# Kernel optimization log

Measured on AMD Instinct MI355X. Metric: run time of the kernel, lower is better.

Reference implementation:

```python
import jax, jax.numpy as jnp
import numpy as np

N, E, IN_D, H, OUT_D = 50000, 800000, 128, 64, 64


def setup_inputs() -> dict:
    key = jax.random.key(0)
    ks = jax.random.split(key, 16)
    s = lambda k, shape: jax.random.normal(k, shape, dtype=jnp.float32) * (1.0 / np.sqrt(shape[0]))
    return {
        "x": jax.random.normal(ks[0], (N, IN_D), dtype=jnp.float32),
        "edge_index": jax.random.randint(ks[1], (2, E), 0, N, dtype=jnp.int32),
        "W1": s(ks[2], (IN_D, H)), "b1": jnp.zeros((H,), jnp.float32),
        "W2": s(ks[3], (H, 2 * H)), "b2": jnp.zeros((2 * H,), jnp.float32),
        "W3": s(ks[4], (2 * H, 4 * H)), "b3": jnp.zeros((4 * H,), jnp.float32),
        "dec1_w": s(ks[5], (4 * H, 2 * H, 2)), "dec1_b": jnp.zeros((2 * H,), jnp.float32),
        "dec2_w": s(ks[6], (2 * H, H, 2)), "dec2_b": jnp.zeros((H,), jnp.float32),
        "dec3_w": s(ks[7], (H, H, 2)), "dec3_b": jnp.zeros((H,), jnp.float32),
        "skip1_w": s(ks[8], (2 * H, 2 * H)), "skip1_b": jnp.zeros((2 * H,), jnp.float32),
        "skip2_w": s(ks[9], (H, H)), "skip2_b": jnp.zeros((H,), jnp.float32),
        "fin_w": s(ks[10], (OUT_D, 8 * H)), "fin_b": jnp.zeros((OUT_D,), jnp.float32),
    }


def _deconv2(x, w, b):
    # ConvTranspose1d(kernel=2, stride=2): [n,c,l] x [c,o,2] -> [n,o,2l]
    y = jnp.einsum('ncl,cok->nolk', x, w)
    n, o = x.shape[0], w.shape[1]
    return y.reshape(n, o, -1) + b[None, :, None]


def reference(x, edge_index, W1, b1, W2, b2, W3, b3, dec1_w, dec1_b, dec2_w, dec2_b,
              dec3_w, dec3_b, skip1_w, skip1_b, skip2_w, skip2_b, fin_w, fin_b):
    n = x.shape[0]
    loop = jnp.arange(n, dtype=edge_index.dtype)
    src = jnp.concatenate([edge_index[0], loop])
    tgt = jnp.concatenate([edge_index[1], loop])
    deg = jax.ops.segment_sum(jnp.ones_like(src, dtype=x.dtype), tgt, num_segments=n)
    dinv = jax.lax.rsqrt(deg)  # deg >= 1 due to self-loops
    norm = dinv[src] * dinv[tgt]  # [E+N]

    def gcn(h, W, b):
        hw = h @ W
        agg = jax.ops.segment_sum(hw[src] * norm[:, None], tgt, num_segments=n)
        return agg + b

    x1 = jax.nn.gelu(gcn(x, W1, b1))    # [N, H]
    x2 = jax.nn.gelu(gcn(x1, W2, b2))   # [N, 2H]
    x3 = jax.nn.gelu(gcn(x2, W3, b3))   # [N, 4H]

    d = _deconv2(x3[:, :, None], dec1_w, dec1_b)           # [N, 2H, 2]
    d = d + (x2 @ skip1_w.T + skip1_b)[:, :, None]
    d = _deconv2(d, dec2_w, dec2_b)                        # [N, H, 4]
    d = d + (x1 @ skip2_w.T + skip2_b)[:, :, None]
    d = _deconv2(d, dec3_w, dec3_b)                        # [N, H, 8]
    out = d.reshape(n, -1) @ fin_w.T + fin_b               # [N, OUT_D]
    return out
```

## Files before the change

kernel.cpp:

```cpp
#include <hip/hip_runtime.h>
#include <hip/hip_bf16.h>

typedef __attribute__((ext_vector_type(8))) short short8_t;
typedef __attribute__((ext_vector_type(4))) float f32x4;

#define CAP 64

__device__ __forceinline__ float gelu_f(float x) {
    float x3 = x * x * x;
    return 0.5f * x * (1.0f + tanhf(0.7978845608028654f * (x + 0.044715f * x3)));
}
__device__ __forceinline__ float b2f(unsigned short u) {
    union { float f; unsigned int i; } c; c.i = ((unsigned int)u) << 16; return c.f;
}
__device__ __forceinline__ unsigned short f2bu(float f) {
    union { float f; unsigned int i; } c; c.f = f;
    unsigned int r = c.i + 0x7fffu + ((c.i >> 16) & 1u);
    return (unsigned short)(r >> 16);
}


__device__ __forceinline__ void d_EF(int bid, int t, const float* __restrict__ dec3_w,
                                     const float* __restrict__ fin_w, float* __restrict__ EF) {
    int i2 = bid * 4 + (t >> 6), od = t & 63;
    int c3 = i2 >> 2, pp = i2 & 3;
    const float* d3 = dec3_w + c3 * 128;
    const float* fw = fin_w + od * 512;
    float s = 0.f;
    #pragma unroll
    for (int o3 = 0; o3 < 64; ++o3) {
        s += d3[o3 * 2 + 0] * fw[o3 * 8 + pp * 2 + 0];
        s += d3[o3 * 2 + 1] * fw[o3 * 8 + pp * 2 + 1];
    }
    EF[i2 * 64 + od] = s;
}

__device__ __forceinline__ void d_CEF(int bid, int t, const float* __restrict__ dec2_w,
                                      const float* __restrict__ EF, float* __restrict__ CEF) {
    int i1 = bid * 4 + (t >> 6), od = t & 63;
    int c2 = i1 >> 1, lp = i1 & 1;
    const float* d2 = dec2_w + c2 * 128;
    float s = 0.f;
    #pragma unroll
    for (int o2 = 0; o2 < 64; ++o2) {
        s += d2[o2 * 2 + 0] * EF[(o2 * 4 + lp * 2 + 0) * 64 + od];
        s += d2[o2 * 2 + 1] * EF[(o2 * 4 + lp * 2 + 1) * 64 + od];
    }
    CEF[i1 * 64 + od] = s;
}

__device__ __forceinline__ void d_comp(int sb, int od,
                       const float* __restrict__ dec1_w, const float* __restrict__ skip1_w,
                       const float* __restrict__ skip2_w,
                       const float* __restrict__ dec1_b, const float* __restrict__ skip1_b,
                       const float* __restrict__ dec2_b, const float* __restrict__ skip2_b,
                       const float* __restrict__ dec3_b, const float* __restrict__ fin_w,
                       const float* __restrict__ fin_b,
                       const float* __restrict__ CEF, const float* __restrict__ EF,
                       unsigned short* __restrict__ McatT, float* __restrict__ m0) {
    if (sb < 256) {
        const float* d1 = dec1_w + sb * 256;
        float s = 0.f;
        for (int j = 0; j < 256; ++j) s += d1[j] * CEF[j * 64 + od];
        McatT[od * 448 + sb] = f2bu(s);
    } else if (sb < 384) {
        int c = sb - 256;
        float s = 0.f;
        for (int j = 0; j < 256; ++j) s += skip1_w[(j >> 1) * 128 + c] * CEF[j * 64 + od];
        McatT[od * 448 + sb] = f2bu(s);
    } else if (sb < 448) {
        int c = sb - 384;
        float s = 0.f;
        for (int j = 0; j < 256; ++j) s += skip2_w[(j >> 2) * 64 + c] * EF[j * 64 + od];
        McatT[od * 448 + sb] = f2bu(s);
    } else {
        float s = fin_b[od];
        for (int j = 0; j < 256; ++j) s += (dec1_b[j >> 1] + skip1_b[j >> 1]) * CEF[j * 64 + od];
        for (int j = 0; j < 256; ++j) s += (dec2_b[j >> 2] + skip2_b[j >> 2]) * EF[j * 64 + od];
        for (int j = 0; j < 512; ++j) s += dec3_b[j >> 3] * fin_w[od * 512 + j];
        m0[od] = s;
    }
}

__device__ __forceinline__ void d_wconv(int bid, int t,
                        const float* __restrict__ W1, const float* __restrict__ W2,
                        const float* __restrict__ W3,
                        unsigned short* __restrict__ W1T, unsigned short* __restrict__ W2T,
                        unsigned short* __restrict__ W3T) {
    int i = bid * 256 + t;
    if (i < 8192) {
        int k = i >> 6, n = i & 63;
        W1T[n * 128 + k] = f2bu(W1[i]);
    } else if (i < 16384) {
        int j = i - 8192; int k = j >> 7, n = j & 127;
        W2T[n * 64 + k] = f2bu(W2[j]);
    } else if (i < 49152) {
        int j = i - 16384; int k = j >> 8, n = j & 255;
        W3T[n * 128 + k] = f2bu(W3[j]);
    }
}

__device__ __forceinline__ void d_fillx(int bid, int t, const int* __restrict__ src,
                                        const int* __restrict__ tgt, int E,
                                        int* __restrict__ cnt, int* __restrict__ csr) {
    int i = (bid * 256 + t) * 8;
    if (i + 7 < E) {
        int4 t0 = *(const int4*)(tgt + i);
        int4 t1 = *(const int4*)(tgt + i + 4);
        int4 s0 = *(const int4*)(src + i);
        int4 s1 = *(const int4*)(src + i + 4);
        int k0 = atomicAdd(&cnt[t0.x], 1);
        int k1 = atomicAdd(&cnt[t0.y], 1);
        int k2 = atomicAdd(&cnt[t0.z], 1);
        int k3 = atomicAdd(&cnt[t0.w], 1);
        int k4 = atomicAdd(&cnt[t1.x], 1);
        int k5 = atomicAdd(&cnt[t1.y], 1);
        int k6 = atomicAdd(&cnt[t1.z], 1);
        int k7 = atomicAdd(&cnt[t1.w], 1);
        if (k0 < CAP) csr[(t0.x << 6) + k0] = s0.x;
        if (k1 < CAP) csr[(t0.y << 6) + k1] = s0.y;
        if (k2 < CAP) csr[(t0.z << 6) + k2] = s0.z;
        if (k3 < CAP) csr[(t0.w << 6) + k3] = s0.w;
        if (k4 < CAP) csr[(t1.x << 6) + k4] = s1.x;
        if (k5 < CAP) csr[(t1.y << 6) + k5] = s1.y;
        if (k6 < CAP) csr[(t1.z << 6) + k6] = s1.z;
        if (k7 < CAP) csr[(t1.w << 6) + k7] = s1.w;
    } else {
        for (int k = i; k < E; ++k) {
            int tt = tgt[k];
            int kk = atomicAdd(&cnt[tt], 1);
            if (kk < CAP) csr[(tt << 6) + kk] = src[k];
        }
    }
}

template<bool A32, bool BIAS, bool GELU, bool OUT32>
__device__ __forceinline__ void d_gmm(
    int bx, int by,
    const unsigned short* __restrict__ A, const float* __restrict__ Af, int lda,
    const unsigned short* __restrict__ Bt,
    const float* __restrict__ bias,
    void* __restrict__ Cv, int ldc, int M, int K) {
    constexpr int LDS_R = 72;
    __shared__ unsigned short As[64 * LDS_R];
    __shared__ unsigned short Bs[64 * LDS_R];
    const int tid = threadIdx.x;
    const int r0 = bx * 64, c0 = by * 64;
    const int w = tid >> 6, lane = tid & 63;
    const int wm = (w >> 1) * 32, wn = (w & 1) * 32;
    const int fr = lane & 15, kg = lane >> 4;
    f32x4 acc[2][2];
    #pragma unroll
    for (int m = 0; m < 2; ++m)
        #pragma unroll
        for (int n = 0; n < 2; ++n) { f32x4 z = {0.f, 0.f, 0.f, 0.f}; acc[m][n] = z; }

    const int sr = tid >> 2, sc = (tid & 3) * 16;
    const bool aok = (r0 + sr) < M;
    const unsigned short* ag = A32 ? nullptr : (A + (size_t)(r0 + sr) * lda + sc);
    const float* agf = A32 ? (Af + (size_t)(r0 + sr) * lda + sc) : nullptr;
    const unsigned short* bg = Bt + (size_t)(c0 + sr) * K + sc;

    for (int kt = 0; kt < K; kt += 64) {
        if (aok) {
            if constexpr (A32) {
                float4 f0 = *(const float4*)(agf + kt);
                float4 f1 = *(const float4*)(agf + kt + 4);
                float4 f2 = *(const float4*)(agf + kt + 8);
                float4 f3 = *(const float4*)(agf + kt + 12);
                unsigned short o[16] = { f2bu(f0.x), f2bu(f0.y), f2bu(f0.z), f2bu(f0.w),
                                         f2bu(f1.x), f2bu(f1.y), f2bu(f1.z), f2bu(f1.w),
                                         f2bu(f2.x), f2bu(f2.y), f2bu(f2.z), f2bu(f2.w),
                                         f2bu(f3.x), f2bu(f3.y), f2bu(f3.z), f2bu(f3.w) };
                *(uint4*)&As[sr * LDS_R + sc]     = ((const uint4*)o)[0];
                *(uint4*)&As[sr * LDS_R + sc + 8] = ((const uint4*)o)[1];
            } else {
                *(uint4*)&As[sr * LDS_R + sc]     = *(const uint4*)(ag + kt);
                *(uint4*)&As[sr * LDS_R + sc + 8] = *(const uint4*)(ag + kt + 8);
            }
        }
        *(uint4*)&Bs[sr * LDS_R + sc]     = *(const uint4*)(bg + kt);
        *(uint4*)&Bs[sr * LDS_R + sc + 8] = *(const uint4*)(bg + kt + 8);
        __syncthreads();
        #pragma unroll
        for (int s2 = 0; s2 < 2; ++s2) {
            short8_t afr[2], bfr[2];
            #pragma unroll
            for (int n = 0; n < 2; ++n)
                bfr[n] = *(const short8_t*)&Bs[(wn + n * 16 + fr) * LDS_R + s2 * 32 + kg * 8];
            #pragma unroll
            for (int m = 0; m < 2; ++m)
                afr[m] = *(const short8_t*)&As[(wm + m * 16 + fr) * LDS_R + s2 * 32 + kg * 8];
            #pragma unroll
            for (int m = 0; m < 2; ++m)
                #pragma unroll
                for (int n = 0; n < 2; ++n)
                    acc[m][n] = __builtin_amdgcn_mfma_f32_16x16x32_bf16(afr[m], bfr[n], acc[m][n], 0, 0, 0);
        }
        __syncthreads();
    }
    #pragma unroll
    for (int m = 0; m < 2; ++m) {
        #pragma unroll
        for (int n = 0; n < 2; ++n) {
            #pragma unroll
            for (int j = 0; j < 4; ++j) {
                int row = r0 + wm + m * 16 + kg * 4 + j;
                int col = c0 + wn + n * 16 + fr;
                if (row < M) {
                    float xv = acc[m][n][j];
                    if (BIAS) xv += bias[col];
                    if (GELU) xv = gelu_f(xv);
                    if (OUT32) ((float*)Cv)[(size_t)row * ldc + col] = xv;
                    else ((unsigned short*)Cv)[(size_t)row * ldc + col] = f2bu(xv);
                }
            }
        }
    }
}

template<int F, int LPN, bool FIRST, bool EPI>
__device__ __forceinline__ void d_aggb(
    int bid,
    const unsigned short* __restrict__ hin, int ldi,
    const int* __restrict__ cnt, const int* __restrict__ csr,
    float* __restrict__ normf,
    const float* __restrict__ bias,
    unsigned short* __restrict__ out, int ldo, int N) {
    constexpr int SLOTS = 64 / LPN;
    static_assert(F / LPN == 8, "V must be 8");
    int lane = threadIdx.x & 63;
    int v = bid * 4 + (threadIdx.x >> 6);
    if (v >= N) return;
    int slot = lane / LPN, fl = lane % LPN;
    int fo = fl * 8;
    int deg = cnt[v];
    float dv = rsqrtf((float)(deg + 1));
    int cntE = min(deg, CAP) + 1;
    int base = v << 6;
    float acc[8] = {};
    const unsigned short* hbase = hin + fo;
    int j = slot;
    for (; j + SLOTS < cntE; j += 2 * SLOTS) {
        int e0 = base + j - 1, e1 = base + j + SLOTS - 1;
        int u0 = (j == 0) ? v : csr[e0];
        int u1 = csr[e1];
        float w0, w1;
        if constexpr (FIRST) {
            w0 = (j == 0) ? dv * dv : rsqrtf((float)(cnt[u0] + 1)) * dv;
            w1 = rsqrtf((float)(cnt[u1] + 1)) * dv;
            if (fl == 0) {
                if (j > 0) normf[e0] = w0;
                normf[e1] = w1;
            }
        } else {
            w0 = (j == 0) ? dv * dv : normf[e0];
            w1 = normf[e1];
        }
        uint4 t0 = *(const uint4*)(hbase + (size_t)u0 * ldi);
        uint4 t1 = *(const uint4*)(hbase + (size_t)u1 * ldi);
        const unsigned short* a0 = (const unsigned short*)&t0;
        const unsigned short* a1 = (const unsigned short*)&t1;
        #pragma unroll
        for (int q = 0; q < 8; ++q) acc[q] = fmaf(b2f(a0[q]), w0, acc[q]);
        #pragma unroll
        for (int q = 0; q < 8; ++q) acc[q] = fmaf(b2f(a1[q]), w1, acc[q]);
    }
    if (j < cntE) {
        int e = base + j - 1;
        int u = (j == 0) ? v : csr[e];
        float wgt;
        if constexpr (FIRST) {
            wgt = (j == 0) ? dv * dv : rsqrtf((float)(cnt[u] + 1)) * dv;
            if (fl == 0 && j > 0) normf[e] = wgt;
        } else {
            wgt = (j == 0) ? dv * dv : normf[e];
        }
        uint4 t = *(const uint4*)(hbase + (size_t)u * ldi);
        const unsigned short* ts = (const unsigned short*)&t;
        #pragma unroll
        for (int q = 0; q < 8; ++q) acc[q] = fmaf(b2f(ts[q]), wgt, acc[q]);
    }
    #pragma unroll
    for (int off = LPN; off < 64; off <<= 1)
        #pragma unroll
        for (int q = 0; q < 8; ++q) acc[q] += __shfl_xor(acc[q], off, 64);
    if (slot == 0) {
        unsigned short o[8];
        #pragma unroll
        for (int q = 0; q < 8; ++q) {
            float xv = acc[q];
            if (EPI) xv = gelu_f(xv + bias[fo + q]);
            o[q] = f2bu(xv);
        }
        *(uint4*)(out + (size_t)v * ldo + fo) = *(const uint4*)o;
    }
}


template<bool A32, bool BIAS, bool GELU, bool OUT32>
__global__ __launch_bounds__(256) void k_gmm(
    const unsigned short* __restrict__ A, const float* __restrict__ Af, int lda,
    const unsigned short* __restrict__ Bt,
    const float* __restrict__ bias,
    void* __restrict__ Cv, int ldc, int M, int K) {
    d_gmm<A32, BIAS, GELU, OUT32>(blockIdx.x, blockIdx.y, A, Af, lda, Bt, bias, Cv, ldc, M, K);
}

template<int F, int LPN, bool FIRST, bool EPI>
__global__ __launch_bounds__(256) void k_aggb(
    const unsigned short* __restrict__ hin, int ldi,
    const int* __restrict__ cnt, const int* __restrict__ csr,
    float* __restrict__ normf, const float* __restrict__ bias,
    unsigned short* __restrict__ out, int ldo, int N) {
    d_aggb<F, LPN, FIRST, EPI>(blockIdx.x, hin, ldi, cnt, csr, normf, bias, out, ldo, N);
}

__global__ __launch_bounds__(256) void k_mega0(
    const float* __restrict__ W1, const float* __restrict__ W2, const float* __restrict__ W3,
    unsigned short* __restrict__ W1T, unsigned short* __restrict__ W2T,
    unsigned short* __restrict__ W3T,
    const float* __restrict__ dec3_w, const float* __restrict__ fin_w, float* __restrict__ EF,
    int* __restrict__ cnt, int N) {
    int b = blockIdx.x, t = threadIdx.x;
    if (b < 192) d_wconv(b, t, W1, W2, W3, W1T, W2T, W3T);
    else if (b < 256) d_EF(b - 192, t, dec3_w, fin_w, EF);
    else { int i = (b - 256) * 256 + t; if (i < N) cnt[i] = 0; }
}

__global__ __launch_bounds__(256) void k_megaA(
    const int* __restrict__ src, const int* __restrict__ tgt, int E,
    int* __restrict__ cnt, int* __restrict__ csr, int nf,
    const float* __restrict__ x, const unsigned short* __restrict__ W1T,
    unsigned short* __restrict__ hw1, int M, int ng,
    const float* __restrict__ dec2_w, const float* __restrict__ EF, float* __restrict__ CEF) {
    int b = blockIdx.x;
    if (b < nf)
        d_fillx(b, threadIdx.x, src, tgt, E, cnt, csr);
    else if (b < nf + ng)
        d_gmm<true, false, false, false>(b - nf, 0, nullptr, x, 128, W1T,
                                         (const float*)nullptr, hw1, 64, M, 128);
    else
        d_CEF(b - nf - ng, threadIdx.x, dec2_w, EF, CEF);
}

__global__ __launch_bounds__(256) void k_megaB(
    const unsigned short* __restrict__ hw1,
    const int* __restrict__ cnt, const int* __restrict__ csr, float* __restrict__ normf,
    const float* __restrict__ b1, unsigned short* __restrict__ x1out, int N, int na,
    const float* __restrict__ dec1_w, const float* __restrict__ skip1_w,
    const float* __restrict__ skip2_w,
    const float* __restrict__ dec1_b, const float* __restrict__ skip1_b,
    const float* __restrict__ dec2_b, const float* __restrict__ skip2_b,
    const float* __restrict__ dec3_b, const float* __restrict__ fin_w,
    const float* __restrict__ fin_b,
    const float* __restrict__ CEF, const float* __restrict__ EF,
    unsigned short* __restrict__ McatT, float* __restrict__ m0) {
    int b = blockIdx.x, t = threadIdx.x;
    if (b < na) {
        d_aggb<64, 8, true, true>(b, hw1, 64, cnt, csr, normf, b1, x1out, 448, N);
    } else {
        int sb = (b - na) * 4 + (t >> 6);
        if (sb <= 448)
            d_comp(sb, t & 63, dec1_w, skip1_w, skip2_w, dec1_b, skip1_b, dec2_b, skip2_b,
                   dec3_b, fin_w, fin_b, CEF, EF, McatT, m0);
    }
}

extern "C" void kernel_launch(void* const* d_in, const int* in_sizes, int n_in,
                              void* d_out, int out_size, void* d_ws, size_t ws_size,
                              hipStream_t stream) {
    const float* x       = (const float*)d_in[0];
    const int*   ei      = (const int*)d_in[1];
    const float* W1      = (const float*)d_in[2];
    const float* b1      = (const float*)d_in[3];
    const float* W2      = (const float*)d_in[4];
    const float* b2      = (const float*)d_in[5];
    const float* W3      = (const float*)d_in[6];
    const float* b3      = (const float*)d_in[7];
    const float* dec1_w  = (const float*)d_in[8];
    const float* dec1_b  = (const float*)d_in[9];
    const float* dec2_w  = (const float*)d_in[10];
    const float* dec2_b  = (const float*)d_in[11];
    const float* dec3_w  = (const float*)d_in[12];
    const float* dec3_b  = (const float*)d_in[13];
    const float* skip1_w = (const float*)d_in[14];
    const float* skip1_b = (const float*)d_in[15];
    const float* skip2_w = (const float*)d_in[16];
    const float* skip2_b = (const float*)d_in[17];
    const float* fin_w   = (const float*)d_in[18];
    const float* fin_b   = (const float*)d_in[19];

    const int N = in_sizes[0] / 128;
    const int E = in_sizes[1] / 2;
    const int* e_src = ei;
    const int* e_tgt = ei + E;

    char* p = (char*)d_ws;
    auto alloc = [&](size_t bytes) -> void* {
        void* r = p;
        p += (bytes + 255) & ~(size_t)255;
        return r;
    };
    int*   cnt     = (int*)alloc((size_t)N * 4);
    int*   csr     = (int*)alloc((size_t)N * CAP * 4);
    float* normf   = (float*)alloc((size_t)N * CAP * 4);
    float* EF      = (float*)alloc(256 * 64 * 4);
    float* CEF     = (float*)alloc(256 * 64 * 4);
    float* m0      = (float*)alloc(64 * 4);
    unsigned short* McatT = (unsigned short*)alloc(64 * 448 * 2);
    unsigned short* W1T   = (unsigned short*)alloc(64 * 128 * 2);
    unsigned short* W2T   = (unsigned short*)alloc(128 * 64 * 2);
    unsigned short* W3T   = (unsigned short*)alloc(256 * 128 * 2);
    unsigned short* hw1   = (unsigned short*)alloc((size_t)N * 64 * 2);
    unsigned short* a1    = (unsigned short*)alloc((size_t)N * 64 * 2);
    unsigned short* xcat  = (unsigned short*)alloc((size_t)N * 448 * 2);
    unsigned short* a2    = hw1;
    if ((size_t)(p - (char*)d_ws) > ws_size) return;

    const int nf = (E / 8 + 255) / 256;
    const int mg = (N + 63) / 64;
    const int ag = (N + 3) / 4;
    const int compb = (449 + 3) / 4;
    const int zb = (N + 255) / 256;

    k_mega0<<<dim3(192 + 64 + zb), dim3(256), 0, stream>>>(
        W1, W2, W3, W1T, W2T, W3T, dec3_w, fin_w, EF, cnt, N);

    k_megaA<<<dim3(nf + mg + 64), dim3(256), 0, stream>>>(
        e_src, e_tgt, E, cnt, csr, nf, x, W1T, hw1, N, mg, dec2_w, EF, CEF);

    k_megaB<<<dim3(ag + compb), dim3(256), 0, stream>>>(
        hw1, cnt, csr, normf, b1, xcat + 384, N, ag,
        dec1_w, skip1_w, skip2_w, dec1_b, skip1_b, dec2_b, skip2_b, dec3_b,
        fin_w, fin_b, CEF, EF, McatT, m0);

    k_aggb<64, 8, false, false><<<dim3(ag), dim3(256), 0, stream>>>(
        xcat + 384, 448, cnt, csr, normf, (const float*)nullptr, a1, 64, N);
    k_gmm<false, true, true, false><<<dim3(mg, 2), dim3(256), 0, stream>>>(
        a1, nullptr, 64, W2T, b2, xcat + 256, 448, N, 64);

    k_aggb<128, 16, false, false><<<dim3(ag), dim3(256), 0, stream>>>(
        xcat + 256, 448, cnt, csr, normf, (const float*)nullptr, a2, 128, N);
    k_gmm<false, true, true, false><<<dim3(mg, 4), dim3(256), 0, stream>>>(
        a2, nullptr, 128, W3T, b3, xcat, 448, N, 128);

    k_gmm<false, true, false, true><<<dim3(mg, 1), dim3(256), 0, stream>>>(
        xcat, nullptr, 448, McatT, m0, d_out, 64, N, 448);
}
```

Measured before the change: 218.8 us.

## Factor symmetric GCN normalization into pre-scaled features, dropping per-edge norm array

New measurement: 220.4 us. No clear change (+0.8%).

```diff
diff --git a/kernel.cpp b/kernel.cpp
--- a/kernel.cpp
+++ b/kernel.cpp
@@ -134,13 +134,14 @@
     }
 }
 
-template<bool A32, bool BIAS, bool GELU, bool OUT32>
+template<bool A32, bool BIAS, bool GELU, bool OUT32, bool GX>
 __device__ __forceinline__ void d_gmm(
     int bx, int by,
     const unsigned short* __restrict__ A, const float* __restrict__ Af, int lda,
     const unsigned short* __restrict__ Bt,
     const float* __restrict__ bias,
-    void* __restrict__ Cv, int ldc, int M, int K) {
+    void* __restrict__ Cv, int ldc, int M, int K,
+    const float* __restrict__ dinvp, unsigned short* __restrict__ gxp, int ldg) {
     constexpr int LDS_R = 72;
     __shared__ unsigned short As[64 * LDS_R];
     __shared__ unsigned short Bs[64 * LDS_R];
@@ -213,20 +214,22 @@
                     if (GELU) xv = gelu_f(xv);
                     if (OUT32) ((float*)Cv)[(size_t)row * ldc + col] = xv;
                     else ((unsigned short*)Cv)[(size_t)row * ldc + col] = f2bu(xv);
+                    if (GX) gxp[(size_t)row * ldg + col] = f2bu(dinvp[row] * xv);
                 }
             }
         }
     }
 }
 
-template<int F, int LPN, bool FIRST, bool EPI>
+template<int F, int LPN, bool EPI>
 __device__ __forceinline__ void d_aggb(
     int bid,
-    const unsigned short* __restrict__ hin, int ldi,
+    const unsigned short* __restrict__ g, int ldi,
+    const float* __restrict__ dinv,
     const int* __restrict__ cnt, const int* __restrict__ csr,
-    float* __restrict__ normf,
     const float* __restrict__ bias,
-    unsigned short* __restrict__ out, int ldo, int N) {
+    unsigned short* __restrict__ out, int ldo,
+    unsigned short* __restrict__ gxout, int ldg, int N) {
     constexpr int SLOTS = 64 / LPN;
     static_assert(F / LPN == 8, "V must be 8");
     int lane = threadIdx.x & 63;
@@ -234,52 +237,30 @@
     if (v >= N) return;
     int slot = lane / LPN, fl = lane % LPN;
     int fo = fl * 8;
-    int deg = cnt[v];
-    float dv = rsqrtf((float)(deg + 1));
-    int cntE = min(deg, CAP) + 1;
+    float dv = dinv[v];
+    int cntE = min(cnt[v], CAP) + 1;
     int base = v << 6;
     float acc[8] = {};
-    const unsigned short* hbase = hin + fo;
+    const unsigned short* hbase = g + fo;
     int j = slot;
     for (; j + SLOTS < cntE; j += 2 * SLOTS) {
-        int e0 = base + j - 1, e1 = base + j + SLOTS - 1;
-        int u0 = (j == 0) ? v : csr[e0];
-        int u1 = csr[e1];
-        float w0, w1;
-        if constexpr (FIRST) {
-            w0 = (j == 0) ? dv * dv : rsqrtf((float)(cnt[u0] + 1)) * dv;
-            w1 = rsqrtf((float)(cnt[u1] + 1)) * dv;
-            if (fl == 0) {
-                if (j > 0) normf[e0] = w0;
-                normf[e1] = w1;
-            }
-        } else {
-            w0 = (j == 0) ? dv * dv : normf[e0];
-            w1 = normf[e1];
-        }
+        int u0 = (j == 0) ? v : csr[base + j - 1];
+        int u1 = csr[base + j + SLOTS - 1];
         uint4 t0 = *(const uint4*)(hbase + (size_t)u0 * ldi);
         uint4 t1 = *(const uint4*)(hbase + (size_t)u1 * ldi);
         const unsigned short* a0 = (const unsigned short*)&t0;
         const unsigned short* a1 = (const unsigned short*)&t1;
         #pragma unroll
-        for (int q = 0; q < 8; ++q) acc[q] = fmaf(b2f(a0[q]), w0, acc[q]);
-        #pragma unroll
-        for (int q = 0; q < 8; ++q) acc[q] = fmaf(b2f(a1[q]), w1, acc[q]);
+        for (int q = 0; q < 8; ++q) acc[q] += b2f(a0[q]);
+        #pragma unroll
+        for (int q = 0; q < 8; ++q) acc[q] += b2f(a1[q]);
     }
     if (j < cntE) {
-        int e = base + j - 1;
-        int u = (j == 0) ? v : csr[e];
-        float wgt;
-        if constexpr (FIRST) {
-            wgt = (j == 0) ? dv * dv : rsqrtf((float)(cnt[u] + 1)) * dv;
-            if (fl == 0 && j > 0) normf[e] = wgt;
-        } else {
-            wgt = (j == 0) ? dv * dv : normf[e];
-        }
+        int u = (j == 0) ? v : csr[base + j - 1];
         uint4 t = *(const uint4*)(hbase + (size_t)u * ldi);
         const unsigned short* ts = (const unsigned short*)&t;
         #pragma unroll
-        for (int q = 0; q < 8; ++q) acc[q] = fmaf(b2f(ts[q]), wgt, acc[q]);
+        for (int q = 0; q < 8; ++q) acc[q] += b2f(ts[q]);
     }
     #pragma unroll
     for (int off = LPN; off < 64; off <<= 1)
@@ -287,33 +268,58 @@
         for (int q = 0; q < 8; ++q) acc[q] += __shfl_xor(acc[q], off, 64);
     if (slot == 0) {
         unsigned short o[8];
+        unsigned short o2[8];
         #pragma unroll
         for (int q = 0; q < 8; ++q) {
-            float xv = acc[q];
-            if (EPI) xv = gelu_f(xv + bias[fo + q]);
+            float xv = dv * acc[q];
+            if (EPI) {
+                xv = gelu_f(xv + bias[fo + q]);
+                o2[q] = f2bu(dv * xv);
+            }
             o[q] = f2bu(xv);
         }
         *(uint4*)(out + (size_t)v * ldo + fo) = *(const uint4*)o;
-    }
-}
-
-
-template<bool A32, bool BIAS, bool GELU, bool OUT32>
+        if (EPI) *(uint4*)(gxout + (size_t)v * ldg + fo) = *(const uint4*)o2;
+    }
+}
+
+
+template<bool A32, bool BIAS, bool GELU, bool OUT32, bool GX>
 __global__ __launch_bounds__(256) void k_gmm(
     const unsigned short* __restrict__ A, const float* __restrict__ Af, int lda,
     const unsigned short* __restrict__ Bt,
     const float* __restrict__ bias,
-    void* __restrict__ Cv, int ldc, int M, int K) {
-    d_gmm<A32, BIAS, GELU, OUT32>(blockIdx.x, blockIdx.y, A, Af, lda, Bt, bias, Cv, ldc, M, K);
-}
-
-template<int F, int LPN, bool FIRST, bool EPI>
+    void* __restrict__ Cv, int ldc, int M, int K,
+    const float* __restrict__ dinvp, unsigned short* __restrict__ gxp, int ldg) {
+    d_gmm<A32, BIAS, GELU, OUT32, GX>(blockIdx.x, blockIdx.y, A, Af, lda, Bt, bias,
+                                      Cv, ldc, M, K, dinvp, gxp, ldg);
+}
+
+template<int F, int LPN, bool EPI>
 __global__ __launch_bounds__(256) void k_aggb(
-    const unsigned short* __restrict__ hin, int ldi,
+    const unsigned short* __restrict__ g, int ldi,
+    const float* __restrict__ dinv,
     const int* __restrict__ cnt, const int* __restrict__ csr,
-    float* __restrict__ normf, const float* __restrict__ bias,
-    unsigned short* __restrict__ out, int ldo, int N) {
-    d_aggb<F, LPN, FIRST, EPI>(blockIdx.x, hin, ldi, cnt, csr, normf, bias, out, ldo, N);
+    const float* __restrict__ bias,
+    unsigned short* __restrict__ out, int ldo,
+    unsigned short* __restrict__ gxout, int ldg, int N) {
+    d_aggb<F, LPN, EPI>(blockIdx.x, g, ldi, dinv, cnt, csr, bias, out, ldo, gxout, ldg, N);
+}
+
+__global__ __launch_bounds__(256) void k_scale(
+    const int* __restrict__ cnt, unsigned short* __restrict__ g,
+    float* __restrict__ dinv, int N) {
+    int i = blockIdx.x * 256 + threadIdx.x;
+    if (i >= N * 8) return;
+    int v = i >> 3;
+    float dv = rsqrtf((float)(cnt[v] + 1));
+    if ((i & 7) == 0) dinv[v] = dv;
+    uint4 h = ((const uint4*)g)[i];
+    const unsigned short* hs = (const unsigned short*)&h;
+    unsigned short o[8];
+    #pragma unroll
+    for (int q = 0; q < 8; ++q) o[q] = f2bu(b2f(hs[q]) * dv);
+    ((uint4*)g)[i] = *(const uint4*)o;
 }
 
 __global__ __launch_bounds__(256) void k_mega0(
@@ -338,16 +344,19 @@
     if (b < nf)
         d_fillx(b, threadIdx.x, src, tgt, E, cnt, csr);
     else if (b < nf + ng)
-        d_gmm<true, false, false, false>(b - nf, 0, nullptr, x, 128, W1T,
-                                         (const float*)nullptr, hw1, 64, M, 128);
+        d_gmm<true, false, false, false, false>(b - nf, 0, nullptr, x, 128, W1T,
+                                                (const float*)nullptr, hw1, 64, M, 128,
+                                                nullptr, nullptr, 0);
     else
         d_CEF(b - nf - ng, threadIdx.x, dec2_w, EF, CEF);
 }
 
 __global__ __launch_bounds__(256) void k_megaB(
-    const unsigned short* __restrict__ hw1,
-    const int* __restrict__ cnt, const int* __restrict__ csr, float* __restrict__ normf,
-    const float* __restrict__ b1, unsigned short* __restrict__ x1out, int N, int na,
+    const unsigned short* __restrict__ g1,
+    const float* __restrict__ dinv,
+    const int* __restrict__ cnt, const int* __restrict__ csr,
+    const float* __restrict__ b1, unsigned short* __restrict__ x1out,
+    unsigned short* __restrict__ gx1, int N, int na,
     const float* __restrict__ dec1_w, const float* __restrict__ skip1_w,
     const float* __restrict__ skip2_w,
     const float* __restrict__ dec1_b, const float* __restrict__ skip1_b,
@@ -358,7 +367,7 @@
     unsigned short* __restrict__ McatT, float* __restrict__ m0) {
     int b = blockIdx.x, t = threadIdx.x;
     if (b < na) {
-        d_aggb<64, 8, true, true>(b, hw1, 64, cnt, csr, normf, b1, x1out, 448, N);
+        d_aggb<64, 8, true>(b, g1, 64, dinv, cnt, csr, b1, x1out, 448, gx1, 64, N);
     } else {
         int sb = (b - na) * 4 + (t >> 6);
         if (sb <= 448)
@@ -404,7 +413,7 @@
     };
     int*   cnt     = (int*)alloc((size_t)N * 4);
     int*   csr     = (int*)alloc((size_t)N * CAP * 4);
-    float* normf   = (float*)alloc((size_t)N * CAP * 4);
+    float* dinv    = (float*)alloc((size_t)N * 4);
     float* EF      = (float*)alloc(256 * 64 * 4);
     float* CEF     = (float*)alloc(256 * 64 * 4);
     float* m0      = (float*)alloc(64 * 4);
@@ -414,6 +423,7 @@
     unsigned short* W3T   = (unsigned short*)alloc(256 * 128 * 2);
     unsigned short* hw1   = (unsigned short*)alloc((size_t)N * 64 * 2);
     unsigned short* a1    = (unsigned short*)alloc((size_t)N * 64 * 2);
+    unsigned short* gx    = (unsigned short*)alloc((size_t)N * 128 * 2);
     unsigned short* xcat  = (unsigned short*)alloc((size_t)N * 448 * 2);
     unsigned short* a2    = hw1;
     if ((size_t)(p - (char*)d_ws) > ws_size) return;
@@ -423,6 +433,7 @@
     const int ag = (N + 3) / 4;
     const int compb = (449 + 3) / 4;
     const int zb = (N + 255) / 256;
+    const int sb = (N * 8 + 255) / 256;
 
     k_mega0<<<dim3(192 + 64 + zb), dim3(256), 0, stream>>>(
         W1, W2, W3, W1T, W2T, W3T, dec3_w, fin_w, EF, cnt, N);
@@ -430,21 +441,23 @@
     k_megaA<<<dim3(nf + mg + 64), dim3(256), 0, stream>>>(
         e_src, e_tgt, E, cnt, csr, nf, x, W1T, hw1, N, mg, dec2_w, EF, CEF);
 
+    k_scale<<<dim3(sb), dim3(256), 0, stream>>>(cnt, hw1, dinv, N);
+
     k_megaB<<<dim3(ag + compb), dim3(256), 0, stream>>>(
-        hw1, cnt, csr, normf, b1, xcat + 384, N, ag,
+        hw1, dinv, cnt, csr, b1, xcat + 384, gx, N, ag,
         dec1_w, skip1_w, skip2_w, dec1_b, skip1_b, dec2_b, skip2_b, dec3_b,
         fin_w, fin_b, CEF, EF, McatT, m0);
 
-    k_aggb<64, 8, false, false><<<dim3(ag), dim3(256), 0, stream>>>(
-        xcat + 384, 448, cnt, csr, normf, (const float*)nullptr, a1, 64, N);
-    k_gmm<false, true, true, false><<<dim3(mg, 2), dim3(256), 0, stream>>>(
-        a1, nullptr, 64, W2T, b2, xcat + 256, 448, N, 64);
-
-    k_aggb<128, 16, false, false><<<dim3(ag), dim3(256), 0, stream>>>(
-        xcat + 256, 448, cnt, csr, normf, (const float*)nullptr, a2, 128, N);
-    k_gmm<false, true, true, false><<<dim3(mg, 4), dim3(256), 0, stream>>>(
-        a2, nullptr, 128, W3T, b3, xcat, 448, N, 128);
-
-    k_gmm<false, true, false, true><<<dim3(mg, 1), dim3(256), 0, stream>>>(
-        xcat, nullptr, 448, McatT, m0, d_out, 64, N, 448);
-}
+    k_aggb<64, 8, false><<<dim3(ag), dim3(256), 0, stream>>>(
+        gx, 64, dinv, cnt, csr, (const float*)nullptr, a1, 64, nullptr, 0, N);
+    k_gmm<false, true, true, false, true><<<dim3(mg, 2), dim3(256), 0, stream>>>(
+        a1, nullptr, 64, W2T, b2, xcat + 256, 448, N, 64, dinv, gx, 128);
+
+    k_aggb<128, 16, false><<<dim3(ag), dim3(256), 0, stream>>>(
+        gx, 128, dinv, cnt, csr, (const float*)nullptr, a2, 128, nullptr, 0, N);
+    k_gmm<false, true, true, false, false><<<dim3(mg, 4), dim3(256), 0, stream>>>(
+        a2, nullptr, 128, W3T, b3, xcat, 448, N, 128, nullptr, nullptr, 0);
+
+    k_gmm<false, true, false, true, false><<<dim3(mg, 1), dim3(256), 0, stream>>>(
+        xcat, nullptr, 448, McatT, m0, d_out, 64, N, 448, nullptr, nullptr, 0);
+}
```
